# Kernel optimization log

Hardware: AMD Instinct MI355X
Metric: run time of the kernel (lower is better)

The kernel has to match this reference:

```python
import jax, jax.numpy as jnp
import numpy as np

USER_NUM = 100000
ITEM_NUM = 50000
N = USER_NUM + ITEM_NUM
D = 64
NNZ = 2400000
B = 4096
NLEVEL = 3
LEAF = 32
HID = 256
NCLS = 2
NLAYERS = 2
EPS = 0.1
TAU = 0.2


def _l2norm(x, axis=-1):
    return x / jnp.clip(jnp.linalg.norm(x, axis=axis, keepdims=True), 1e-12)


def setup_inputs():
    key = jax.random.key(0)
    ks = jax.random.split(key, 32)
    def w(k, shape):
        fan = shape[-2] if len(shape) >= 2 else shape[-1]
        return jax.random.normal(k, shape, jnp.float32) / np.sqrt(fan)
    z = lambda *s: jnp.zeros(s, jnp.float32)
    return {
        "ego_emb": w(ks[0], (N, D)),
        "gc_w": w(ks[1], (NLAYERS, D, D)), "gc_b": z(NLAYERS, D),
        "bi_w": w(ks[2], (NLAYERS, D, D)), "bi_b": z(NLAYERS, D),
        "uh_w": w(ks[3], (NLEVEL, D, D)), "uh_b": z(NLEVEL, D),
        "ih_w": w(ks[4], (NLEVEL, D, D)), "ih_b": z(NLEVEL, D),
        "ud_w1": w(ks[5], (NLEVEL, D, HID)), "ud_b1": z(NLEVEL, HID),
        "ud_w2": w(ks[6], (NLEVEL, HID, LEAF)), "ud_b2": z(NLEVEL, LEAF),
        "id_w1": w(ks[7], (NLEVEL, D, HID)), "id_b1": z(NLEVEL, HID),
        "id_w2": w(ks[8], (NLEVEL, HID, LEAF)), "id_b2": z(NLEVEL, LEAF),
        "q_w": w(ks[9], (LEAF, LEAF)), "q_b": z(LEAF),
        "k_w": w(ks[10], (LEAF, LEAF)), "k_b": z(LEAF),
        "v_w": w(ks[11], (LEAF, LEAF)), "v_b": z(LEAF),
        "dg_w1": w(ks[12], (NLEVEL * LEAF, D)), "dg_b1": z(D),
        "dg_w2": w(ks[13], (D, D)), "dg_b2": z(D),
        "pr_w": w(ks[14], (D, NCLS)), "pr_b": z(NCLS),
        "adj_vals": jax.random.uniform(ks[15], (NNZ,), jnp.float32) / 16.0,
        "hier_skills": jax.random.uniform(ks[16], (B, NLEVEL * LEAF), jnp.float32),
        "user_id": jax.random.randint(ks[17], (B,), 0, USER_NUM),
        "item_id": jax.random.randint(ks[18], (B,), 0, ITEM_NUM),
        "adj_rows": jax.random.randint(ks[19], (NNZ,), 0, N),
        "adj_cols": jax.random.randint(ks[20], (NNZ,), 0, N),
    }


def _sam(x, q_w, q_b, k_w, k_b, v_w, v_b):
    # x: [B, S, d], single-head self-attention (n_heads=1)
    d = x.shape[-1]
    q = x @ q_w + q_b
    k = x @ k_w + k_b
    v = x @ v_w + v_b
    scores = jnp.einsum('bsd,btd->bst', q, k) / jnp.sqrt(jnp.float32(d))
    attn = jax.nn.softmax(scores, axis=-1)  # softmax over key axis t
    return jnp.einsum('bst,btd->bsd', attn, v)


def _cl_loss(v1, v2):
    n1 = _l2norm(v1)
    n2 = _l2norm(v2)
    pos = jnp.exp(jnp.sum(n1 * n2, -1) / TAU)
    ttl = jnp.sum(jnp.exp(n1 @ n2.T / TAU), axis=1)
    return jnp.mean(-jnp.log(pos / ttl))


def _cl_module(recs, key):
    # recs: [L, B, LEAF]
    noise = jax.random.uniform(key, recs.shape, recs.dtype)
    recs_new = recs + jnp.sign(recs) * _l2norm(noise) * EPS
    return jnp.mean(jax.vmap(_cl_loss)(recs, recs_new))


def reference(ego_emb, gc_w, gc_b, bi_w, bi_b, uh_w, uh_b, ih_w, ih_b,
              ud_w1, ud_b1, ud_w2, ud_b2, id_w1, id_b1, id_w2, id_b2,
              q_w, q_b, k_w, k_b, v_w, v_b, dg_w1, dg_b1, dg_w2, dg_b2,
              pr_w, pr_b, adj_vals, hier_skills, user_id, item_id,
              adj_rows, adj_cols):
    # ---- NGCF propagation: sparse adj matmul + bi-interaction ----
    E = ego_emb
    E_sum = ego_emb
    for l in range(NLAYERS):
        side = jax.ops.segment_sum(adj_vals[:, None] * E[adj_cols], adj_rows,
                                   num_segments=N)  # spmm(adj_norm, E)
        sum_e = jax.nn.leaky_relu(side @ gc_w[l] + gc_b[l])
        bi_e = jax.nn.leaky_relu((E * side) @ bi_w[l] + bi_b[l])
        E = _l2norm(sum_e + bi_e)  # dropout -> identity (eval)
        E_sum = E_sum + E
    ue = E_sum[:USER_NUM][user_id]   # [B, D]
    ie = E_sum[USER_NUM:][item_id]   # [B, D]
    # ---- hierarchy projections + disentangled encoders (stacked over levels) ----
    u_reps = jnp.tanh(jnp.einsum('bd,lde->lbe', ue, uh_w) + uh_b[:, None, :])
    i_reps = jnp.tanh(jnp.einsum('bd,lde->lbe', ie, ih_w) + ih_b[:, None, :])
    u_recs = jnp.einsum('lbh,lhk->lbk',
                        jnp.tanh(jnp.einsum('lbd,ldh->lbh', u_reps, ud_w1) + ud_b1[:, None, :]),
                        ud_w2) + ud_b2[:, None, :]  # [L, B, LEAF]
    i_recs = jnp.einsum('lbh,lhk->lbk',
                        jnp.tanh(jnp.einsum('lbd,ldh->lbh', i_reps, id_w1) + id_b1[:, None, :]),
                        id_w2) + id_b2[:, None, :]
    # ---- self-attention across levels ----
    u_att = _sam(u_recs.transpose(1, 0, 2), q_w, q_b, k_w, k_b, v_w, v_b)  # [B, L, LEAF]
    i_att = _sam(i_recs.transpose(1, 0, 2), q_w, q_b, k_w, k_b, v_w, v_b)
    # ---- contrastive losses (detached in original via torch.Tensor(...)) ----
    kc = jax.random.split(jax.random.key(42), 2)
    cl = _cl_module(u_att.transpose(1, 0, 2), kc[0]) + _cl_module(i_att.transpose(1, 0, 2), kc[1])
    cl = jax.lax.stop_gradient(cl)
    # ---- diagnosis head ----
    skills = hier_skills.reshape(B, NLEVEL, LEAF)
    diag = ((jax.nn.sigmoid(u_att) - jax.nn.sigmoid(i_att)) * skills).reshape(B, NLEVEL * LEAF)
    h = jnp.tanh(diag @ dg_w1 + dg_b1) @ dg_w2 + dg_b2  # dropout -> identity (eval)
    out = jax.nn.softmax(h @ pr_w + pr_b, axis=-1)
    return (out, cl)
```

## Files before the change

### kernel.cpp

```cpp
#include <hip/hip_runtime.h>
#include <stdint.h>
#include <math.h>

#define USER_N 100000
#define NODE_N 150000
#define DD 64
#define NNZE 2400000
#define BB 4096
#define NLV 3
#define LF 32
#define HALF_SZ 196608u
#define NTILE 586
#define NSUB 8
#define SCAP 1024
#define EPB 4096
#define LCAP 5120

typedef __attribute__((ext_vector_type(8))) short bf16x8;
typedef __attribute__((ext_vector_type(4))) float f32x4;
typedef __attribute__((ext_vector_type(2))) float f32x2;

#define XCC_ID_IMM 63508

__host__ __device__ inline void tf_block(uint32_t k0, uint32_t k1, uint32_t& x0, uint32_t& x1) {
  uint32_t ks[3] = {k0, k1, k0 ^ k1 ^ 0x1BD11BDAu};
  x0 += ks[0]; x1 += ks[1];
  const int R0[4] = {13, 15, 26, 6};
  const int R1[4] = {17, 29, 16, 24};
#pragma unroll
  for (int i = 0; i < 5; ++i) {
    const int* R = (i & 1) ? R1 : R0;
#pragma unroll
    for (int j = 0; j < 4; ++j) {
      x0 += x1;
      x1 = (x1 << R[j]) | (x1 >> (32 - R[j]));
      x1 ^= x0;
    }
    x0 += ks[(i + 1) % 3];
    x1 += ks[(i + 2) % 3] + (uint32_t)(i + 1);
  }
}

__device__ inline float tf_uniform(uint32_t ka, uint32_t kb, uint32_t m) {
  uint32_t x0, x1;
  bool first = m < HALF_SZ;
  if (first) { x0 = m; x1 = m + HALF_SZ; } else { x0 = m - HALF_SZ; x1 = m; }
  tf_block(ka, kb, x0, x1);
  uint32_t bits = first ? x0 : x1;
  return __uint_as_float((bits >> 9) | 0x3f800000u) - 1.0f;
}

__device__ inline unsigned short f2bf(float x) {
  uint32_t b = __float_as_uint(x);
  return (unsigned short)((b + 0x7FFFu + ((b >> 16) & 1u)) >> 16);
}

__device__ inline unsigned char f2fp8(float x) {
  return (unsigned char)(__builtin_amdgcn_cvt_pk_fp8_f32(x, x, 0, false) & 0xFF);
}

__device__ inline void fp8_fma(float4& acc, uint2 rec, uint32_t wrd) {
  float vv = __uint_as_float(rec.y);
  f32x2 lo = __builtin_amdgcn_cvt_pk_f32_fp8((int)wrd, false);
  f32x2 hi = __builtin_amdgcn_cvt_pk_f32_fp8((int)wrd, true);
  acc.x = fmaf(vv, lo.x, acc.x);
  acc.y = fmaf(vv, lo.y, acc.y);
  acc.z = fmaf(vv, hi.x, acc.z);
  acc.w = fmaf(vv, hi.y, acc.w);
}

__global__ __launch_bounds__(256) void k_init(
    const float* __restrict__ ego, uint32_t* __restrict__ E8,
    const float* __restrict__ uh_w, const float* __restrict__ ud_w1,
    const float* __restrict__ ud_w2, const float* __restrict__ ih_w,
    const float* __restrict__ id_w1, const float* __restrict__ id_w2,
    unsigned short* __restrict__ s1t, unsigned short* __restrict__ s2t,
    unsigned short* __restrict__ s3t) {
  if (blockIdx.x < 9375) {
    int i = blockIdx.x * 256 + threadIdx.x;
    float4 v = ((const float4*)ego)[i];
    int w01 = __builtin_amdgcn_cvt_pk_fp8_f32(v.x, v.y, 0, false);
    int w = __builtin_amdgcn_cvt_pk_fp8_f32(v.z, v.w, w01, true);
    E8[i] = (uint32_t)w;
    return;
  }
  int i = (blockIdx.x - 9375) * 256 + threadIdx.x;
  if (i < 24576) {
    int sl = i >> 12, r = i & 4095, e = r >> 6, d = r & 63;
    const float* src = (sl >= 3 ? ih_w : uh_w);
    int l = sl % 3;
    s1t[i] = f2bf(src[l * 4096 + d * 64 + e]);
  } else if (i < 24576 + 98304) {
    int j = i - 24576;
    int sl = j >> 14, r = j & 16383, e = r >> 6, d = r & 63;
    const float* src = (sl >= 3 ? id_w1 : ud_w1);
    int l = sl % 3;
    s2t[j] = f2bf(src[l * 16384 + d * 256 + e]);
  } else if (i < 172032) {
    int j = i - 24576 - 98304;
    int sl = j >> 13, r = j & 8191, e = r >> 8, d = r & 255;
    const float* src = (sl >= 3 ? id_w2 : ud_w2);
    int l = sl % 3;
    s3t[j] = f2bf(src[l * 8192 + d * 32 + e]);
  }
}

__global__ __launch_bounds__(256) void k_scatter_t(const int* __restrict__ rows,
                                                   const int* __restrict__ cols,
                                                   const float* __restrict__ vals,
                                                   int* __restrict__ cursor,
                                                   uint2* __restrict__ sedge_r) {
  __shared__ int cnt[NTILE];
  __shared__ int binbase[NTILE];
  __shared__ int gbase[NTILE];
  __shared__ int partial[256];
  __shared__ uint2 staged[EPB];
  __shared__ unsigned short tileof[EPB];
  int t = threadIdx.x;
  for (int i = t; i < NTILE; i += 256) cnt[i] = 0;
  __syncthreads();
  int ebase = blockIdx.x * EPB;
  int r[16], rk[16];
#pragma unroll
  for (int j = 0; j < 16; ++j) {
    int e = ebase + j * 256 + t;
    r[j] = (e < NNZE) ? rows[e] : -1;
    rk[j] = (r[j] >= 0) ? atomicAdd(&cnt[r[j] >> 8], 1) : 0;
  }
  __syncthreads();
  int b0 = t * 3;
  int own = (b0 < NTILE) ? ((NTILE - b0 < 3) ? (NTILE - b0) : 3) : 0;
  int s0 = 0;
  for (int k = 0; k < own; ++k) s0 += cnt[b0 + k];
  partial[t] = s0;
  __syncthreads();
  for (int off = 1; off < 256; off <<= 1) {
    int add = (t >= off) ? partial[t - off] : 0;
    __syncthreads();
    partial[t] += add;
    __syncthreads();
  }
  int excl = partial[t] - s0;
  unsigned myx = __builtin_amdgcn_s_getreg(XCC_ID_IMM) & (NSUB - 1);
  {
    int run = excl;
    for (int k = 0; k < own; ++k) {
      int b = b0 + k;
      int c = cnt[b];
      binbase[b] = run;
      gbase[b] = c ? atomicAdd(&cursor[(b * NSUB + (int)myx) * 16], c) : 0;
      run += c;
    }
  }
  __syncthreads();
#pragma unroll
  for (int j = 0; j < 16; ++j) {
    if (r[j] < 0) continue;
    int e = ebase + j * 256 + t;
    int tile = r[j] >> 8;
    int pos = binbase[tile] + rk[j];
    staged[pos] = make_uint2((uint32_t)cols[e] | ((uint32_t)(r[j] & 255) << 18),
                             __float_as_uint(vals[e]));
    tileof[pos] = (unsigned short)tile;
  }
  __syncthreads();
  int nrec = NNZE - ebase;
  if (nrec > EPB) nrec = EPB;
  for (int i = t; i < nrec; i += 256) {
    int tile = tileof[i];
    int q = i - binbase[tile];
    int p = gbase[tile] + q;
    uint2 rec = staged[i];
    if (p < SCAP) {
      sedge_r[(size_t)(tile * NSUB + (int)myx) * SCAP + p] = rec;
    } else {
#pragma unroll 1
      for (int att = 1; att < NSUB; ++att) {
        int seg = tile * NSUB + (int)((myx + att) & (NSUB - 1));
        int p2 = atomicAdd(&cursor[seg * 16], 1);
        if (p2 < SCAP) { sedge_r[(size_t)seg * SCAP + p2] = rec; break; }
      }
    }
  }
}

__global__ __launch_bounds__(256) void k_sort_t(const uint2* __restrict__ sedge_r,
                                                const int* __restrict__ cursor,
                                                uint2* __restrict__ sedge,
                                                int* __restrict__ row_start) {
  __shared__ int hist[256], buf[256], curs[256];
  __shared__ int obase_s;
  __shared__ uint2 staged[LCAP];
  int t = threadIdx.x;
  int tile = blockIdx.x;
  if (t == 0) obase_s = 0;
  hist[t] = 0;
  __syncthreads();
  int ob = 0;
  for (int i = t; i < tile * NSUB; i += 256) {
    int c = cursor[i * 16];
    ob += (c < SCAP) ? c : SCAP;
  }
  if (ob) atomicAdd(&obase_s, ob);
  int segcnt[NSUB];
#pragma unroll
  for (int x = 0; x < NSUB; ++x) {
    int c = cursor[(tile * NSUB + x) * 16];
    segcnt[x] = (c < SCAP) ? c : SCAP;
  }
#pragma unroll 1
  for (int x = 0; x < NSUB; ++x) {
    const uint2* sp = sedge_r + (size_t)(tile * NSUB + x) * SCAP;
    for (int i = t; i < segcnt[x]; i += 256)
      atomicAdd(&hist[sp[i].x >> 18], 1);
  }
  __syncthreads();
  int obase = obase_s;
  int v = hist[t];
  buf[t] = v;
  __syncthreads();
  for (int off = 1; off < 256; off <<= 1) {
    int add = (t >= off) ? buf[t - off] : 0;
    __syncthreads();
    buf[t] += add;
    __syncthreads();
  }
  int total = buf[255];
  int excl = buf[t] - v;
  curs[t] = excl;
  int row = tile * 256 + t;
  if (row < NODE_N) row_start[row] = obase + excl;
  if (tile == NTILE - 1 && t == 0) row_start[NODE_N] = NNZE;
  __syncthreads();
#pragma unroll 1
  for (int x = 0; x < NSUB; ++x) {
    const uint2* sp = sedge_r + (size_t)(tile * NSUB + x) * SCAP;
    for (int i = t; i < segcnt[x]; i += 256) {
      uint2 rec = sp[i];
      int rl = rec.x >> 18;
      int p = atomicAdd(&curs[rl], 1);
      uint2 outrec = make_uint2(rec.x & 0x3FFFFu, rec.y);
      if (p < LCAP) staged[p] = outrec;
      else sedge[obase + p] = outrec;
    }
  }
  __syncthreads();
  int n = (total < LCAP) ? total : LCAP;
  for (int i = t; i < n; i += 256)
    sedge[obase + i] = staged[i];
}

__global__ __launch_bounds__(256) void k_spmm(const uint32_t* __restrict__ E8,
                                              const uint2* __restrict__ sedge,
                                              const int* __restrict__ row_start,
                                              unsigned short* __restrict__ side16,
                                              unsigned short* __restrict__ p16) {
  int r = blockIdx.x * 4 + (threadIdx.x >> 6);
  int lane = threadIdx.x & 63;
  int g = lane >> 4;
  int q = lane & 15;
  int rs = row_start[r], re = row_start[r + 1];
  float4 acc = make_float4(0.f, 0.f, 0.f, 0.f);
  int e = rs;
  for (; e + 16 <= re; e += 16) {
    uint2 e0 = sedge[e + g];
    uint2 e1 = sedge[e + 4 + g];
    uint2 e2 = sedge[e + 8 + g];
    uint2 e3 = sedge[e + 12 + g];
    uint32_t a0 = E8[(size_t)e0.x * 16 + q];
    uint32_t a1 = E8[(size_t)e1.x * 16 + q];
    uint32_t a2 = E8[(size_t)e2.x * 16 + q];
    uint32_t a3 = E8[(size_t)e3.x * 16 + q];
    fp8_fma(acc, e0, a0);
    fp8_fma(acc, e1, a1);
    fp8_fma(acc, e2, a2);
    fp8_fma(acc, e3, a3);
  }
  for (; e + 8 <= re; e += 8) {
    uint2 e0 = sedge[e + g];
    uint2 e1 = sedge[e + 4 + g];
    uint32_t a0 = E8[(size_t)e0.x * 16 + q];
    uint32_t a1 = E8[(size_t)e1.x * 16 + q];
    fp8_fma(acc, e0, a0);
    fp8_fma(acc, e1, a1);
  }
  for (; e + 4 <= re; e += 4) {
    uint2 e0 = sedge[e + g];
    uint32_t a0 = E8[(size_t)e0.x * 16 + q];
    fp8_fma(acc, e0, a0);
  }
  for (; e < re; ++e) {
    if (g == (e & 3)) {
      uint2 e0 = sedge[e];
      uint32_t a0 = E8[(size_t)e0.x * 16 + q];
      fp8_fma(acc, e0, a0);
    }
  }
#pragma unroll
  for (int off = 16; off <= 32; off <<= 1) {
    acc.x += __shfl_xor(acc.x, off, 64);
    acc.y += __shfl_xor(acc.y, off, 64);
    acc.z += __shfl_xor(acc.z, off, 64);
    acc.w += __shfl_xor(acc.w, off, 64);
  }
  if (g == 0) {
    uint32_t ew = E8[(size_t)r * 16 + q];
    f32x2 elo = __builtin_amdgcn_cvt_pk_f32_fp8((int)ew, false);
    f32x2 ehi = __builtin_amdgcn_cvt_pk_f32_fp8((int)ew, true);
    ushort4 s16, pp;
    s16.x = f2bf(acc.x); s16.y = f2bf(acc.y); s16.z = f2bf(acc.z); s16.w = f2bf(acc.w);
    pp.x = f2bf(acc.x * elo.x); pp.y = f2bf(acc.y * elo.y);
    pp.z = f2bf(acc.z * ehi.x); pp.w = f2bf(acc.w * ehi.y);
    *(ushort4*)&side16[(size_t)r * DD + q * 4] = s16;
    *(ushort4*)&p16[(size_t)r * DD + q * 4] = pp;
  }
}

__global__ __launch_bounds__(256) void k_transform(const float* __restrict__ gw,
                                                   const float* __restrict__ gb,
                                                   const float* __restrict__ bw,
                                                   const float* __restrict__ bb,
                                                   const unsigned short* __restrict__ side16,
                                                   const unsigned short* __restrict__ p16,
                                                   float* __restrict__ Eout,
                                                   unsigned char* __restrict__ E8b) {
  int t = threadIdx.x;
  int wv = t >> 6, lane = t & 63;
  int n = lane & 15, quad = lane >> 4;
  bf16x8 wg[4][2], wb[4][2];
  float gbl[4], bbl[4];
#pragma unroll
  for (int c = 0; c < 4; ++c) {
    gbl[c] = gb[c * 16 + n];
    bbl[c] = bb[c * 16 + n];
#pragma unroll
    for (int h = 0; h < 2; ++h) {
#pragma unroll
      for (int j = 0; j < 8; ++j) {
        int k = h * 32 + quad * 8 + j;
        wg[c][h][j] = (short)f2bf(gw[k * 64 + c * 16 + n]);
        wb[c][h][j] = (short)f2bf(bw[k * 64 + c * 16 + n]);
      }
    }
  }
  const f32x4 z = {0.f, 0.f, 0.f, 0.f};
  for (int tile = blockIdx.x * 4 + wv; tile < NODE_N / 16; tile += gridDim.x * 4) {
    int i0 = tile * 16;
    bf16x8 as0 = *(const bf16x8*)&side16[(size_t)(i0 + n) * DD + quad * 8];
    bf16x8 as1 = *(const bf16x8*)&side16[(size_t)(i0 + n) * DD + 32 + quad * 8];
    bf16x8 ap0 = *(const bf16x8*)&p16[(size_t)(i0 + n) * DD + quad * 8];
    bf16x8 ap1 = *(const bf16x8*)&p16[(size_t)(i0 + n) * DD + 32 + quad * 8];
    float v[4][4];
    float sq0 = 0.f, sq1 = 0.f, sq2 = 0.f, sq3 = 0.f;
#pragma unroll
    for (int c = 0; c < 4; ++c) {
      f32x4 ag = __builtin_amdgcn_mfma_f32_16x16x32_bf16(as0, wg[c][0], z, 0, 0, 0);
      ag = __builtin_amdgcn_mfma_f32_16x16x32_bf16(as1, wg[c][1], ag, 0, 0, 0);
      f32x4 ab = __builtin_amdgcn_mfma_f32_16x16x32_bf16(ap0, wb[c][0], z, 0, 0, 0);
      ab = __builtin_amdgcn_mfma_f32_16x16x32_bf16(ap1, wb[c][1], ab, 0, 0, 0);
#pragma unroll
      for (int r = 0; r < 4; ++r) {
        float a1 = ag[r] + gbl[c];
        a1 = (a1 > 0.f) ? a1 : 0.01f * a1;
        float a2 = ab[r] + bbl[c];
        a2 = (a2 > 0.f) ? a2 : 0.01f * a2;
        float vv = a1 + a2;
        v[c][r] = vv;
        if (r == 0) sq0 += vv * vv;
        else if (r == 1) sq1 += vv * vv;
        else if (r == 2) sq2 += vv * vv;
        else sq3 += vv * vv;
      }
    }
#pragma unroll
    for (int off = 1; off < 16; off <<= 1) {
      sq0 += __shfl_xor(sq0, off, 64);
      sq1 += __shfl_xor(sq1, off, 64);
      sq2 += __shfl_xor(sq2, off, 64);
      sq3 += __shfl_xor(sq3, off, 64);
    }
    float inv0 = 1.f / fmaxf(sqrtf(sq0), 1e-12f);
    float inv1 = 1.f / fmaxf(sqrtf(sq1), 1e-12f);
    float inv2 = 1.f / fmaxf(sqrtf(sq2), 1e-12f);
    float inv3 = 1.f / fmaxf(sqrtf(sq3), 1e-12f);
#pragma unroll
    for (int c = 0; c < 4; ++c) {
      float vn0 = v[c][0] * inv0;
      float vn1 = v[c][1] * inv1;
      float vn2 = v[c][2] * inv2;
      float vn3 = v[c][3] * inv3;
      size_t o0 = (size_t)(i0 + quad * 4 + 0) * DD + c * 16 + n;
      size_t o1 = o0 + DD, o2 = o1 + DD, o3 = o2 + DD;
      Eout[o0] = vn0; Eout[o1] = vn1; Eout[o2] = vn2; Eout[o3] = vn3;
      E8b[o0] = f2fp8(vn0); E8b[o1] = f2fp8(vn1);
      E8b[o2] = f2fp8(vn2); E8b[o3] = f2fp8(vn3);
    }
  }
}

__global__ __launch_bounds__(128) void k_gather(const float* __restrict__ ego,
                                                const float* __restrict__ E1,
                                                const float* __restrict__ E2,
                                                const int* __restrict__ uid,
                                                const int* __restrict__ iid,
                                                unsigned short* __restrict__ ue16,
                                                unsigned short* __restrict__ ie16) {
  int b = blockIdx.x, t = threadIdx.x;
  if (t < 64) {
    size_t o = (size_t)uid[b] * 64 + t;
    ue16[(size_t)b * 64 + t] = f2bf(ego[o] + E1[o] + E2[o]);
  } else {
    int d = t - 64;
    size_t o = (size_t)(USER_N + iid[b]) * 64 + d;
    ie16[(size_t)b * 64 + d] = f2bf(ego[o] + E1[o] + E2[o]);
  }
}

__global__ __launch_bounds__(256) void k_encoder5(
    const unsigned short* __restrict__ ue16, const unsigned short* __restrict__ ie16,
    const unsigned short* __restrict__ s1t, const unsigned short* __restrict__ s2t,
    const unsigned short* __restrict__ s3t,
    const float* __restrict__ uh_b, const float* __restrict__ ud_b1,
    const float* __restrict__ ud_b2, const float* __restrict__ ih_b,
    const float* __restrict__ id_b1, const float* __restrict__ id_b2,
    float* __restrict__ recs_u, float* __restrict__ recs_i) {
  __shared__ unsigned short R1[32][64];
  __shared__ unsigned short T[32][256];
  int t = threadIdx.x;
  int w = t >> 6, lane = t & 63;
  int n = lane & 15, quad = lane >> 4;
  int trow = w & 1;
  int cg = w >> 1;
  int r0 = blockIdx.x * 32;
  int l = blockIdx.y, side = blockIdx.z;
  int sl = side * 3 + l;
  const unsigned short* x16 = side ? ie16 : ue16;
  const float* hb = side ? ih_b : uh_b;
  const float* bb1 = side ? id_b1 : ud_b1;
  const float* bb2 = side ? id_b2 : ud_b2;
  float* recs = side ? recs_i : recs_u;
  const f32x4 z = {0.f, 0.f, 0.f, 0.f};

  {
    const unsigned short* xr = &x16[(size_t)(r0 + trow * 16 + n) * 64];
    bf16x8 a0 = *(const bf16x8*)&xr[quad * 8];
    bf16x8 a1 = *(const bf16x8*)&xr[32 + quad * 8];
    const unsigned short* Wt = s1t + (size_t)sl * 4096;
#pragma unroll
    for (int cc = 0; cc < 2; ++cc) {
      int cb = cg * 2 + cc;
      bf16x8 wb0 = *(const bf16x8*)&Wt[(size_t)(cb * 16 + n) * 64 + quad * 8];
      bf16x8 wb1 = *(const bf16x8*)&Wt[(size_t)(cb * 16 + n) * 64 + 32 + quad * 8];
      f32x4 acc = __builtin_amdgcn_mfma_f32_16x16x32_bf16(a0, wb0, z, 0, 0, 0);
      acc = __builtin_amdgcn_mfma_f32_16x16x32_bf16(a1, wb1, acc, 0, 0, 0);
      float bias = hb[l * 64 + cb * 16 + n];
#pragma unroll
      for (int r = 0; r < 4; ++r)
        R1[trow * 16 + quad * 4 + r][cb * 16 + n] = f2bf(tanhf(acc[r] + bias));
    }
  }
  __syncthreads();

  {
    bf16x8 a0 = *(const bf16x8*)&R1[trow * 16 + n][quad * 8];
    bf16x8 a1 = *(const bf16x8*)&R1[trow * 16 + n][32 + quad * 8];
    const unsigned short* Wt = s2t + (size_t)sl * 16384;
#pragma unroll
    for (int cc = 0; cc < 8; ++cc) {
      int cb = cg * 8 + cc;
      bf16x8 wb0 = *(const bf16x8*)&Wt[(size_t)(cb * 16 + n) * 64 + quad * 8];
      bf16x8 wb1 = *(const bf16x8*)&Wt[(size_t)(cb * 16 + n) * 64 + 32 + quad * 8];
      f32x4 acc = __builtin_amdgcn_mfma_f32_16x16x32_bf16(a0, wb0, z, 0, 0, 0);
      acc = __builtin_amdgcn_mfma_f32_16x16x32_bf16(a1, wb1, acc, 0, 0, 0);
      float bias = bb1[l * 256 + cb * 16 + n];
#pragma unroll
      for (int r = 0; r < 4; ++r)
        T[trow * 16 + quad * 4 + r][cb * 16 + n] = f2bf(tanhf(acc[r] + bias));
    }
  }
  __syncthreads();

  {
    const unsigned short* Wt = s3t + (size_t)sl * 8192;
    f32x4 acc = z;
#pragma unroll
    for (int h = 0; h < 8; ++h) {
      bf16x8 a = *(const bf16x8*)&T[trow * 16 + n][h * 32 + quad * 8];
      bf16x8 b = *(const bf16x8*)&Wt[(size_t)(cg * 16 + n) * 256 + h * 32 + quad * 8];
      acc = __builtin_amdgcn_mfma_f32_16x16x32_bf16(a, b, acc, 0, 0, 0);
    }
    float bias = bb2[l * 32 + cg * 16 + n];
#pragma unroll
    for (int r = 0; r < 4; ++r)
      recs[((size_t)l * BB + (r0 + trow * 16 + quad * 4 + r)) * 32 + cg * 16 + n] =
          acc[r] + bias;
  }
}

__global__ __launch_bounds__(256) void k_attn(const float* __restrict__ recs_u,
                                              const float* __restrict__ recs_i,
                                              const float* __restrict__ qw, const float* __restrict__ qb,
                                              const float* __restrict__ kw, const float* __restrict__ kb,
                                              const float* __restrict__ vw, const float* __restrict__ vb,
                                              float* __restrict__ att_u,
                                              float* __restrict__ att_i) {
  const float* recs = blockIdx.y ? recs_i : recs_u;
  float* att = blockIdx.y ? att_i : att_u;
  int t = threadIdx.x;
  int b = blockIdx.x * 8 + (t >> 5);
  int d = t & 31;
  float x0 = recs[((size_t)0 * BB + b) * 32 + d];
  float x1 = recs[((size_t)1 * BB + b) * 32 + d];
  float x2 = recs[((size_t)2 * BB + b) * 32 + d];
  float q0 = qb[d], q1 = q0, q2 = q0;
  float c0 = kb[d], c1 = c0, c2 = c0;
  float v0 = vb[d], v1 = v0, v2 = v0;
#pragma unroll 4
  for (int kk = 0; kk < 32; ++kk) {
    float xa = __shfl(x0, kk, 32);
    float xb = __shfl(x1, kk, 32);
    float xc = __shfl(x2, kk, 32);
    float wq = qw[kk * 32 + d], wk = kw[kk * 32 + d], wv = vw[kk * 32 + d];
    q0 += xa * wq; q1 += xb * wq; q2 += xc * wq;
    c0 += xa * wk; c1 += xb * wk; c2 += xc * wk;
    v0 += xa * wv; v1 += xb * wv; v2 += xc * wv;
  }
  float qs[3] = {q0, q1, q2}, ks[3] = {c0, c1, c2}, vs[3] = {v0, v1, v2};
  float sc[3][3];
#pragma unroll
  for (int s = 0; s < 3; ++s)
#pragma unroll
    for (int u = 0; u < 3; ++u) {
      float p = qs[s] * ks[u];
#pragma unroll
      for (int off = 16; off; off >>= 1) p += __shfl_xor(p, off, 32);
      sc[s][u] = p * 0.17677669529663687f;
    }
#pragma unroll
  for (int s = 0; s < 3; ++s) {
    float m = fmaxf(sc[s][0], fmaxf(sc[s][1], sc[s][2]));
    float e0 = __expf(sc[s][0] - m), e1 = __expf(sc[s][1] - m), e2 = __expf(sc[s][2] - m);
    float inv = 1.f / (e0 + e1 + e2);
    att[(size_t)b * 96 + s * 32 + d] = (e0 * vs[0] + e1 * vs[1] + e2 * vs[2]) * inv;
  }
}

__global__ __launch_bounds__(256) void k_noise(const float* __restrict__ att_u,
                                               const float* __restrict__ att_i,
                                               uint32_t ku0, uint32_t ku1, uint32_t ki0, uint32_t ki1,
                                               unsigned short* __restrict__ n1b,
                                               unsigned short* __restrict__ n2b,
                                               float* __restrict__ posdot) {
  int t = threadIdx.x;
  int g = blockIdx.x * 8 + (t >> 5);
  int k = t & 31;
  int side = g / (NLV * BB);
  int rem = g - side * (NLV * BB);
  int l = rem >> 12;
  int b = rem & 4095;
  const float* att = side ? att_i : att_u;
  uint32_t ka = side ? ki0 : ku0;
  uint32_t kb = side ? ki1 : ku1;
  float r = att[(size_t)b * 96 + l * 32 + k];
  float ss = r * r;
#pragma unroll
  for (int off = 16; off; off >>= 1) ss += __shfl_xor(ss, off, 32);
  float v1 = r / fmaxf(sqrtf(ss), 1e-12f);
  uint32_t m = ((uint32_t)(l * BB + b)) * 32u + (uint32_t)k;
  float u = tf_uniform(ka, kb, m);
  float us = u * u;
#pragma unroll
  for (int off = 16; off; off >>= 1) us += __shfl_xor(us, off, 32);
  float un = u / fmaxf(sqrtf(us), 1e-12f);
  float sgn = (r > 0.f) ? 1.f : ((r < 0.f) ? -1.f : 0.f);
  float rn = r + sgn * un * 0.1f;
  float s2 = rn * rn;
#pragma unroll
  for (int off = 16; off; off >>= 1) s2 += __shfl_xor(s2, off, 32);
  float v2 = rn / fmaxf(sqrtf(s2), 1e-12f);
  float pd = v1 * v2;
#pragma unroll
  for (int off = 16; off; off >>= 1) pd += __shfl_xor(pd, off, 32);
  size_t o = (size_t)g * 32 + k;
  n1b[o] = f2bf(v1);
  n2b[o] = f2bf(v2);
  if (k == 0) posdot[g] = pd;
}

__global__ __launch_bounds__(256) void k_ttl(const unsigned short* __restrict__ n1b,
                                             const unsigned short* __restrict__ n2b,
                                             float* __restrict__ ttl) {
  int t = threadIdx.x;
  int wv = t >> 6, lane = t & 63;
  int sl = blockIdx.x >> 6;
  int istripe = blockIdx.x & 63;
  int i0 = istripe * 64 + wv * 16;
  const unsigned short* ab = n1b + (size_t)sl * BB * 32;
  const unsigned short* bb = n2b + (size_t)sl * BB * 32;
  int m = lane & 15, quad = lane >> 4;
  bf16x8 afrag = *(const bf16x8*)&ab[(size_t)(i0 + m) * 32 + quad * 8];
  float r0a = 0.f, r1a = 0.f, r2a = 0.f, r3a = 0.f;
  f32x4 z = {0.f, 0.f, 0.f, 0.f};
  for (int jt = 0; jt < 256; jt += 4) {
    bf16x8 b0 = *(const bf16x8*)&bb[((size_t)((jt + 0) * 16 + m)) * 32 + quad * 8];
    bf16x8 b1 = *(const bf16x8*)&bb[((size_t)((jt + 1) * 16 + m)) * 32 + quad * 8];
    bf16x8 b2 = *(const bf16x8*)&bb[((size_t)((jt + 2) * 16 + m)) * 32 + quad * 8];
    bf16x8 b3 = *(const bf16x8*)&bb[((size_t)((jt + 3) * 16 + m)) * 32 + quad * 8];
    f32x4 s0 = __builtin_amdgcn_mfma_f32_16x16x32_bf16(afrag, b0, z, 0, 0, 0);
    f32x4 s1 = __builtin_amdgcn_mfma_f32_16x16x32_bf16(afrag, b1, z, 0, 0, 0);
    f32x4 s2 = __builtin_amdgcn_mfma_f32_16x16x32_bf16(afrag, b2, z, 0, 0, 0);
    f32x4 s3 = __builtin_amdgcn_mfma_f32_16x16x32_bf16(afrag, b3, z, 0, 0, 0);
    r0a += __expf(s0.x * 5.f) + __expf(s1.x * 5.f) + __expf(s2.x * 5.f) + __expf(s3.x * 5.f);
    r1a += __expf(s0.y * 5.f) + __expf(s1.y * 5.f) + __expf(s2.y * 5.f) + __expf(s3.y * 5.f);
    r2a += __expf(s0.z * 5.f) + __expf(s1.z * 5.f) + __expf(s2.z * 5.f) + __expf(s3.z * 5.f);
    r3a += __expf(s0.w * 5.f) + __expf(s1.w * 5.f) + __expf(s2.w * 5.f) + __expf(s3.w * 5.f);
  }
#pragma unroll
  for (int off = 1; off < 16; off <<= 1) {
    r0a += __shfl_xor(r0a, off, 64);
    r1a += __shfl_xor(r1a, off, 64);
    r2a += __shfl_xor(r2a, off, 64);
    r3a += __shfl_xor(r3a, off, 64);
  }
  if (m == 0) {
    int rbase = sl * BB + i0 + quad * 4;
    ttl[rbase + 0] = r0a;
    ttl[rbase + 1] = r1a;
    ttl[rbase + 2] = r2a;
    ttl[rbase + 3] = r3a;
  }
}

__global__ __launch_bounds__(1024) void k_clred(const float* __restrict__ ttl,
                                                const float* __restrict__ posdot,
                                                float* __restrict__ outp) {
  __shared__ float red[1024];
  int t = threadIdx.x;
  float a = 0.f;
  for (int idx = t; idx < 6 * BB; idx += 1024)
    a += logf(ttl[idx]) - posdot[idx] * 5.0f;
  red[t] = a;
  __syncthreads();
  for (int off = 512; off; off >>= 1) {
    if (t < off) red[t] += red[t + off];
    __syncthreads();
  }
  if (t == 0) outp[2 * BB] = red[0] * (1.f / 12288.f);
}

__global__ __launch_bounds__(256) void k_head(const float* __restrict__ att_u,
                                              const float* __restrict__ att_i,
                                              const float* __restrict__ skills,
                                              const float* __restrict__ w1, const float* __restrict__ b1,
                                              const float* __restrict__ w2, const float* __restrict__ b2,
                                              const float* __restrict__ pw, const float* __restrict__ pb,
                                              float* __restrict__ outp) {
  __shared__ float diag[4][96], t1[4][64];
  int t = threadIdx.x;
  int w = t >> 6, lane = t & 63;
  int b = blockIdx.x * 4 + w;
  for (int j = lane; j < 96; j += 64) {
    float su = 1.f / (1.f + __expf(-att_u[(size_t)b * 96 + j]));
    float si = 1.f / (1.f + __expf(-att_i[(size_t)b * 96 + j]));
    diag[w][j] = (su - si) * skills[(size_t)b * 96 + j];
  }
  __syncthreads();
  float a = b1[lane];
#pragma unroll 8
  for (int j = 0; j < 96; ++j) a += diag[w][j] * w1[j * 64 + lane];
  t1[w][lane] = tanhf(a);
  __syncthreads();
  float h = b2[lane];
#pragma unroll 8
  for (int kk = 0; kk < 64; ++kk) h += t1[w][kk] * w2[kk * 64 + lane];
  float p0 = h * pw[lane * 2 + 0];
  float p1 = h * pw[lane * 2 + 1];
#pragma unroll
  for (int off = 32; off; off >>= 1) {
    p0 += __shfl_xor(p0, off, 64);
    p1 += __shfl_xor(p1, off, 64);
  }
  if (lane == 0) {
    float l0 = p0 + pb[0], l1 = p1 + pb[1];
    float m = fmaxf(l0, l1);
    float e0 = __expf(l0 - m), e1 = __expf(l1 - m);
    float inv = 1.f / (e0 + e1);
    outp[(size_t)b * 2 + 0] = e0 * inv;
    outp[(size_t)b * 2 + 1] = e1 * inv;
  }
}

extern "C" void kernel_launch(void* const* d_in, const int* in_sizes, int n_in,
                              void* d_out, int out_size, void* d_ws, size_t ws_size,
                              hipStream_t stream) {
  const float* ego    = (const float*)d_in[0];
  const float* gc_w   = (const float*)d_in[1];
  const float* gc_b   = (const float*)d_in[2];
  const float* bi_w   = (const float*)d_in[3];
  const float* bi_b   = (const float*)d_in[4];
  const float* uh_w   = (const float*)d_in[5];
  const float* uh_b   = (const float*)d_in[6];
  const float* ih_w   = (const float*)d_in[7];
  const float* ih_b   = (const float*)d_in[8];
  const float* ud_w1  = (const float*)d_in[9];
  const float* ud_b1  = (const float*)d_in[10];
  const float* ud_w2  = (const float*)d_in[11];
  const float* ud_b2  = (const float*)d_in[12];
  const float* id_w1  = (const float*)d_in[13];
  const float* id_b1  = (const float*)d_in[14];
  const float* id_w2  = (const float*)d_in[15];
  const float* id_b2  = (const float*)d_in[16];
  const float* q_w    = (const float*)d_in[17];
  const float* q_b    = (const float*)d_in[18];
  const float* k_w    = (const float*)d_in[19];
  const float* k_b    = (const float*)d_in[20];
  const float* v_w    = (const float*)d_in[21];
  const float* v_b    = (const float*)d_in[22];
  const float* dg_w1  = (const float*)d_in[23];
  const float* dg_b1  = (const float*)d_in[24];
  const float* dg_w2  = (const float*)d_in[25];
  const float* dg_b2  = (const float*)d_in[26];
  const float* pr_w   = (const float*)d_in[27];
  const float* pr_b   = (const float*)d_in[28];
  const float* adj_vals = (const float*)d_in[29];
  const float* skills = (const float*)d_in[30];
  const int* user_id  = (const int*)d_in[31];
  const int* item_id  = (const int*)d_in[32];
  const int* adj_rows = (const int*)d_in[33];
  const int* adj_cols = (const int*)d_in[34];
  float* outp = (float*)d_out;

  char* w = (char*)d_ws;
  auto alloc = [&](size_t bytes) -> char* {
    char* p = w;
    w += (bytes + 255) & ~(size_t)255;
    return p;
  };
  float* E1     = (float*)alloc((size_t)NODE_N * DD * 4);
  float* E2     = (float*)alloc((size_t)NODE_N * DD * 4);
  uint32_t* E8  = (uint32_t*)alloc((size_t)NODE_N * DD);
  unsigned short* side16 = (unsigned short*)alloc((size_t)NODE_N * DD * 2);
  unsigned short* p16    = (unsigned short*)alloc((size_t)NODE_N * DD * 2);
  uint2* sedge_r= (uint2*)alloc((size_t)NTILE * NSUB * SCAP * 8);
  uint2* sedge  = (uint2*)alloc((size_t)NNZE * 8);
  int*   cursor = (int*)  alloc((size_t)NTILE * NSUB * 16 * 4);
  int*   row_start = (int*)alloc((size_t)(NODE_N + 1) * 4);
  float* posdot = (float*)alloc((size_t)6 * BB * 4);
  float* ttl    = (float*)alloc((size_t)6 * BB * 4);
  unsigned short* s1t = (unsigned short*)alloc((size_t)24576 * 2);
  unsigned short* s2t = (unsigned short*)alloc((size_t)98304 * 2);
  unsigned short* s3t = (unsigned short*)alloc((size_t)49152 * 2);

  char* ap = (char*)sedge_r;
  auto alias = [&](size_t bytes) -> char* {
    char* p = ap;
    ap += (bytes + 255) & ~(size_t)255;
    return p;
  };
  unsigned short* ue16 = (unsigned short*)alias((size_t)BB * 64 * 2);
  unsigned short* ie16 = (unsigned short*)alias((size_t)BB * 64 * 2);
  float* recs_u = (float*)alias((size_t)NLV * BB * 32 * 4);
  float* recs_i = (float*)alias((size_t)NLV * BB * 32 * 4);
  float* att_u  = (float*)alias((size_t)BB * 96 * 4);
  float* att_i  = (float*)alias((size_t)BB * 96 * 4);
  unsigned short* n1b = (unsigned short*)alias((size_t)6 * BB * 32 * 2);
  unsigned short* n2b = (unsigned short*)alias((size_t)6 * BB * 32 * 2);

  uint32_t a0 = 0, a1 = 2, b0 = 1, b1 = 3;
  tf_block(0u, 42u, a0, a1);
  tf_block(0u, 42u, b0, b1);
  uint32_t ku0 = a0, ku1 = b0;
  uint32_t ki0 = a1, ki1 = b1;

  (void)hipMemsetAsync(cursor, 0, (size_t)NTILE * NSUB * 16 * 4, stream);

  k_init<<<9375 + 672, 256, 0, stream>>>(ego, E8, uh_w, ud_w1, ud_w2,
                                         ih_w, id_w1, id_w2, s1t, s2t, s3t);
  k_scatter_t<<<(NNZE + EPB - 1) / EPB, 256, 0, stream>>>(adj_rows, adj_cols, adj_vals,
                                                          cursor, sedge_r);
  k_sort_t<<<NTILE, 256, 0, stream>>>(sedge_r, cursor, sedge, row_start);

  float* Ebufs[2] = {E1, E2};
  for (int l = 0; l < 2; ++l) {
    k_spmm<<<37500, 256, 0, stream>>>(E8, sedge, row_start, side16, p16);
    k_transform<<<1172, 256, 0, stream>>>(gc_w + l * 4096, gc_b + l * 64,
                                          bi_w + l * 4096, bi_b + l * 64,
                                          side16, p16, Ebufs[l], (unsigned char*)E8);
  }

  k_gather<<<4096, 128, 0, stream>>>(ego, E1, E2, user_id, item_id, ue16, ie16);

  dim3 ge(128, 3, 2);
  k_encoder5<<<ge, 256, 0, stream>>>(ue16, ie16, s1t, s2t, s3t,
                                     uh_b, ud_b1, ud_b2, ih_b, id_b1, id_b2,
                                     recs_u, recs_i);

  dim3 ga(512, 2);
  k_attn<<<ga, 256, 0, stream>>>(recs_u, recs_i, q_w, q_b, k_w, k_b, v_w, v_b,
                                 att_u, att_i);

  k_noise<<<3072, 256, 0, stream>>>(att_u, att_i, ku0, ku1, ki0, ki1, n1b, n2b, posdot);

  k_ttl<<<384, 256, 0, stream>>>(n1b, n2b, ttl);
  k_clred<<<1, 1024, 0, stream>>>(ttl, posdot, outp);

  k_head<<<1024, 256, 0, stream>>>(att_u, att_i, skills, dg_w1, dg_b1, dg_w2, dg_b2,
                                   pr_w, pr_b, outp);
}
```

Before: 524.6 us.

## Fuse gather, noise and CL reduction kernels and fold memset into init

Folds the cursor memset and a new CL accumulator reset into extra blocks of the init kernel. The user/item embedding gather moves into the encoder, and the noise/normalisation step moves into the attention kernel. The final CL reduction moves into k_ttl via atomics with a last-block-done counter. This removes four launches and several small intermediate buffers, in exchange for atomic float accumulation order nondeterminism and redundant gathers across the three level blocks.

```diff
diff --git a/kernel.cpp b/kernel.cpp
--- a/kernel.cpp
+++ b/kernel.cpp
@@ -75,7 +75,14 @@
     const float* __restrict__ ud_w2, const float* __restrict__ ih_w,
     const float* __restrict__ id_w1, const float* __restrict__ id_w2,
     unsigned short* __restrict__ s1t, unsigned short* __restrict__ s2t,
-    unsigned short* __restrict__ s3t) {
+    unsigned short* __restrict__ s3t, int* __restrict__ cursor,
+    float* __restrict__ clbuf) {
+  if (blockIdx.x >= 10047) {
+    int i = (blockIdx.x - 10047) * 256 + threadIdx.x;
+    if (i < NTILE * NSUB * 16) cursor[i] = 0;
+    if (i == 0) { clbuf[0] = 0.f; ((int*)clbuf)[1] = 0; }
+    return;
+  }
   if (blockIdx.x < 9375) {
     int i = blockIdx.x * 256 + threadIdx.x;
     float4 v = ((const float4*)ego)[i];
@@ -398,32 +405,17 @@
   }
 }
 
-__global__ __launch_bounds__(128) void k_gather(const float* __restrict__ ego,
-                                                const float* __restrict__ E1,
-                                                const float* __restrict__ E2,
-                                                const int* __restrict__ uid,
-                                                const int* __restrict__ iid,
-                                                unsigned short* __restrict__ ue16,
-                                                unsigned short* __restrict__ ie16) {
-  int b = blockIdx.x, t = threadIdx.x;
-  if (t < 64) {
-    size_t o = (size_t)uid[b] * 64 + t;
-    ue16[(size_t)b * 64 + t] = f2bf(ego[o] + E1[o] + E2[o]);
-  } else {
-    int d = t - 64;
-    size_t o = (size_t)(USER_N + iid[b]) * 64 + d;
-    ie16[(size_t)b * 64 + d] = f2bf(ego[o] + E1[o] + E2[o]);
-  }
-}
-
-__global__ __launch_bounds__(256) void k_encoder5(
-    const unsigned short* __restrict__ ue16, const unsigned short* __restrict__ ie16,
+__global__ __launch_bounds__(256) void k_encoder6(
+    const float* __restrict__ ego, const float* __restrict__ E1,
+    const float* __restrict__ E2, const int* __restrict__ uid,
+    const int* __restrict__ iid,
     const unsigned short* __restrict__ s1t, const unsigned short* __restrict__ s2t,
     const unsigned short* __restrict__ s3t,
     const float* __restrict__ uh_b, const float* __restrict__ ud_b1,
     const float* __restrict__ ud_b2, const float* __restrict__ ih_b,
     const float* __restrict__ id_b1, const float* __restrict__ id_b2,
     float* __restrict__ recs_u, float* __restrict__ recs_i) {
+  __shared__ unsigned short X[32][72];
   __shared__ unsigned short R1[32][64];
   __shared__ unsigned short T[32][256];
   int t = threadIdx.x;
@@ -434,7 +426,6 @@
   int r0 = blockIdx.x * 32;
   int l = blockIdx.y, side = blockIdx.z;
   int sl = side * 3 + l;
-  const unsigned short* x16 = side ? ie16 : ue16;
   const float* hb = side ? ih_b : uh_b;
   const float* bb1 = side ? id_b1 : ud_b1;
   const float* bb2 = side ? id_b2 : ud_b2;
@@ -442,9 +433,21 @@
   const f32x4 z = {0.f, 0.f, 0.f, 0.f};
 
   {
-    const unsigned short* xr = &x16[(size_t)(r0 + trow * 16 + n) * 64];
-    bf16x8 a0 = *(const bf16x8*)&xr[quad * 8];
-    bf16x8 a1 = *(const bf16x8*)&xr[32 + quad * 8];
+    int row = t >> 3;
+    int c0 = (t & 7) * 8;
+    int node = side ? (USER_N + iid[r0 + row]) : uid[r0 + row];
+    const float* pe = ego + (size_t)node * 64 + c0;
+    const float* p1 = E1 + (size_t)node * 64 + c0;
+    const float* p2 = E2 + (size_t)node * 64 + c0;
+#pragma unroll
+    for (int j = 0; j < 8; ++j)
+      X[row][c0 + j] = f2bf(pe[j] + p1[j] + p2[j]);
+  }
+  __syncthreads();
+
+  {
+    bf16x8 a0 = *(const bf16x8*)&X[trow * 16 + n][quad * 8];
+    bf16x8 a1 = *(const bf16x8*)&X[trow * 16 + n][32 + quad * 8];
     const unsigned short* Wt = s1t + (size_t)sl * 4096;
 #pragma unroll
     for (int cc = 0; cc < 2; ++cc) {
@@ -497,15 +500,21 @@
   }
 }
 
-__global__ __launch_bounds__(256) void k_attn(const float* __restrict__ recs_u,
-                                              const float* __restrict__ recs_i,
-                                              const float* __restrict__ qw, const float* __restrict__ qb,
-                                              const float* __restrict__ kw, const float* __restrict__ kb,
-                                              const float* __restrict__ vw, const float* __restrict__ vb,
-                                              float* __restrict__ att_u,
-                                              float* __restrict__ att_i) {
-  const float* recs = blockIdx.y ? recs_i : recs_u;
-  float* att = blockIdx.y ? att_i : att_u;
+__global__ __launch_bounds__(256) void k_attnz(const float* __restrict__ recs_u,
+                                               const float* __restrict__ recs_i,
+                                               const float* __restrict__ qw, const float* __restrict__ qb,
+                                               const float* __restrict__ kw, const float* __restrict__ kb,
+                                               const float* __restrict__ vw, const float* __restrict__ vb,
+                                               uint32_t ku0, uint32_t ku1, uint32_t ki0, uint32_t ki1,
+                                               float* __restrict__ att_u, float* __restrict__ att_i,
+                                               unsigned short* __restrict__ n1b,
+                                               unsigned short* __restrict__ n2b,
+                                               float* __restrict__ posdot) {
+  int side = blockIdx.y;
+  const float* recs = side ? recs_i : recs_u;
+  float* att = side ? att_i : att_u;
+  uint32_t ka = side ? ki0 : ku0;
+  uint32_t kb2 = side ? ki1 : ku1;
   int t = threadIdx.x;
   int b = blockIdx.x * 8 + (t >> 5);
   int d = t & 31;
@@ -541,55 +550,41 @@
     float m = fmaxf(sc[s][0], fmaxf(sc[s][1], sc[s][2]));
     float e0 = __expf(sc[s][0] - m), e1 = __expf(sc[s][1] - m), e2 = __expf(sc[s][2] - m);
     float inv = 1.f / (e0 + e1 + e2);
-    att[(size_t)b * 96 + s * 32 + d] = (e0 * vs[0] + e1 * vs[1] + e2 * vs[2]) * inv;
-  }
-}
-
-__global__ __launch_bounds__(256) void k_noise(const float* __restrict__ att_u,
-                                               const float* __restrict__ att_i,
-                                               uint32_t ku0, uint32_t ku1, uint32_t ki0, uint32_t ki1,
-                                               unsigned short* __restrict__ n1b,
-                                               unsigned short* __restrict__ n2b,
-                                               float* __restrict__ posdot) {
-  int t = threadIdx.x;
-  int g = blockIdx.x * 8 + (t >> 5);
-  int k = t & 31;
-  int side = g / (NLV * BB);
-  int rem = g - side * (NLV * BB);
-  int l = rem >> 12;
-  int b = rem & 4095;
-  const float* att = side ? att_i : att_u;
-  uint32_t ka = side ? ki0 : ku0;
-  uint32_t kb = side ? ki1 : ku1;
-  float r = att[(size_t)b * 96 + l * 32 + k];
-  float ss = r * r;
-#pragma unroll
-  for (int off = 16; off; off >>= 1) ss += __shfl_xor(ss, off, 32);
-  float v1 = r / fmaxf(sqrtf(ss), 1e-12f);
-  uint32_t m = ((uint32_t)(l * BB + b)) * 32u + (uint32_t)k;
-  float u = tf_uniform(ka, kb, m);
-  float us = u * u;
-#pragma unroll
-  for (int off = 16; off; off >>= 1) us += __shfl_xor(us, off, 32);
-  float un = u / fmaxf(sqrtf(us), 1e-12f);
-  float sgn = (r > 0.f) ? 1.f : ((r < 0.f) ? -1.f : 0.f);
-  float rn = r + sgn * un * 0.1f;
-  float s2 = rn * rn;
-#pragma unroll
-  for (int off = 16; off; off >>= 1) s2 += __shfl_xor(s2, off, 32);
-  float v2 = rn / fmaxf(sqrtf(s2), 1e-12f);
-  float pd = v1 * v2;
-#pragma unroll
-  for (int off = 16; off; off >>= 1) pd += __shfl_xor(pd, off, 32);
-  size_t o = (size_t)g * 32 + k;
-  n1b[o] = f2bf(v1);
-  n2b[o] = f2bf(v2);
-  if (k == 0) posdot[g] = pd;
+    float r = (e0 * vs[0] + e1 * vs[1] + e2 * vs[2]) * inv;
+    att[(size_t)b * 96 + s * 32 + d] = r;
+    float ss = r * r;
+#pragma unroll
+    for (int off = 16; off; off >>= 1) ss += __shfl_xor(ss, off, 32);
+    float nv1 = r / fmaxf(sqrtf(ss), 1e-12f);
+    uint32_t mm = ((uint32_t)(s * BB + b)) * 32u + (uint32_t)d;
+    float u = tf_uniform(ka, kb2, mm);
+    float us = u * u;
+#pragma unroll
+    for (int off = 16; off; off >>= 1) us += __shfl_xor(us, off, 32);
+    float un = u / fmaxf(sqrtf(us), 1e-12f);
+    float sgn = (r > 0.f) ? 1.f : ((r < 0.f) ? -1.f : 0.f);
+    float rn = r + sgn * un * 0.1f;
+    float s2 = rn * rn;
+#pragma unroll
+    for (int off = 16; off; off >>= 1) s2 += __shfl_xor(s2, off, 32);
+    float nv2 = rn / fmaxf(sqrtf(s2), 1e-12f);
+    float pd = nv1 * nv2;
+#pragma unroll
+    for (int off = 16; off; off >>= 1) pd += __shfl_xor(pd, off, 32);
+    int g = side * (NLV * BB) + s * BB + b;
+    size_t o = (size_t)g * 32 + d;
+    n1b[o] = f2bf(nv1);
+    n2b[o] = f2bf(nv2);
+    if (d == 0) posdot[g] = pd;
+  }
 }
 
 __global__ __launch_bounds__(256) void k_ttl(const unsigned short* __restrict__ n1b,
                                              const unsigned short* __restrict__ n2b,
-                                             float* __restrict__ ttl) {
+                                             const float* __restrict__ posdot,
+                                             float* __restrict__ clbuf,
+                                             float* __restrict__ outp) {
+  __shared__ float ws[4];
   int t = threadIdx.x;
   int wv = t >> 6, lane = t & 63;
   int sl = blockIdx.x >> 6;
@@ -622,30 +617,29 @@
     r2a += __shfl_xor(r2a, off, 64);
     r3a += __shfl_xor(r3a, off, 64);
   }
+  float part = 0.f;
   if (m == 0) {
     int rbase = sl * BB + i0 + quad * 4;
-    ttl[rbase + 0] = r0a;
-    ttl[rbase + 1] = r1a;
-    ttl[rbase + 2] = r2a;
-    ttl[rbase + 3] = r3a;
-  }
-}
-
-__global__ __launch_bounds__(1024) void k_clred(const float* __restrict__ ttl,
-                                                const float* __restrict__ posdot,
-                                                float* __restrict__ outp) {
-  __shared__ float red[1024];
-  int t = threadIdx.x;
-  float a = 0.f;
-  for (int idx = t; idx < 6 * BB; idx += 1024)
-    a += logf(ttl[idx]) - posdot[idx] * 5.0f;
-  red[t] = a;
-  __syncthreads();
-  for (int off = 512; off; off >>= 1) {
-    if (t < off) red[t] += red[t + off];
-    __syncthreads();
-  }
-  if (t == 0) outp[2 * BB] = red[0] * (1.f / 12288.f);
+    part = (logf(r0a) - posdot[rbase + 0] * 5.0f)
+         + (logf(r1a) - posdot[rbase + 1] * 5.0f)
+         + (logf(r2a) - posdot[rbase + 2] * 5.0f)
+         + (logf(r3a) - posdot[rbase + 3] * 5.0f);
+  }
+#pragma unroll
+  for (int off = 1; off < 64; off <<= 1)
+    part += __shfl_xor(part, off, 64);
+  if (lane == 0) ws[wv] = part;
+  __syncthreads();
+  if (t == 0) {
+    float blk = ws[0] + ws[1] + ws[2] + ws[3];
+    atomicAdd(&clbuf[0], blk);
+    __threadfence();
+    int done = atomicAdd((int*)&clbuf[1], 1);
+    if (done == 383) {
+      float total = atomicAdd(&clbuf[0], 0.0f);
+      outp[2 * BB] = total * (1.f / 12288.f);
+    }
+  }
 }
 
 __global__ __launch_bounds__(256) void k_head(const float* __restrict__ att_u,
@@ -746,7 +740,7 @@
   int*   cursor = (int*)  alloc((size_t)NTILE * NSUB * 16 * 4);
   int*   row_start = (int*)alloc((size_t)(NODE_N + 1) * 4);
   float* posdot = (float*)alloc((size_t)6 * BB * 4);
-  float* ttl    = (float*)alloc((size_t)6 * BB * 4);
+  float* clbuf  = (float*)alloc(256);
   unsigned short* s1t = (unsigned short*)alloc((size_t)24576 * 2);
   unsigned short* s2t = (unsigned short*)alloc((size_t)98304 * 2);
   unsigned short* s3t = (unsigned short*)alloc((size_t)49152 * 2);
@@ -757,8 +751,6 @@
     ap += (bytes + 255) & ~(size_t)255;
     return p;
   };
-  unsigned short* ue16 = (unsigned short*)alias((size_t)BB * 64 * 2);
-  unsigned short* ie16 = (unsigned short*)alias((size_t)BB * 64 * 2);
   float* recs_u = (float*)alias((size_t)NLV * BB * 32 * 4);
   float* recs_i = (float*)alias((size_t)NLV * BB * 32 * 4);
   float* att_u  = (float*)alias((size_t)BB * 96 * 4);
@@ -772,10 +764,9 @@
   uint32_t ku0 = a0, ku1 = b0;
   uint32_t ki0 = a1, ki1 = b1;
 
-  (void)hipMemsetAsync(cursor, 0, (size_t)NTILE * NSUB * 16 * 4, stream);
-
-  k_init<<<9375 + 672, 256, 0, stream>>>(ego, E8, uh_w, ud_w1, ud_w2,
-                                         ih_w, id_w1, id_w2, s1t, s2t, s3t);
+  k_init<<<10341, 256, 0, stream>>>(ego, E8, uh_w, ud_w1, ud_w2,
+                                    ih_w, id_w1, id_w2, s1t, s2t, s3t,
+                                    cursor, clbuf);
   k_scatter_t<<<(NNZE + EPB - 1) / EPB, 256, 0, stream>>>(adj_rows, adj_cols, adj_vals,
                                                           cursor, sedge_r);
   k_sort_t<<<NTILE, 256, 0, stream>>>(sedge_r, cursor, sedge, row_start);
@@ -788,21 +779,18 @@
                                           side16, p16, Ebufs[l], (unsigned char*)E8);
   }
 
-  k_gather<<<4096, 128, 0, stream>>>(ego, E1, E2, user_id, item_id, ue16, ie16);
-
   dim3 ge(128, 3, 2);
-  k_encoder5<<<ge, 256, 0, stream>>>(ue16, ie16, s1t, s2t, s3t,
+  k_encoder6<<<ge, 256, 0, stream>>>(ego, E1, E2, user_id, item_id,
+                                     s1t, s2t, s3t,
                                      uh_b, ud_b1, ud_b2, ih_b, id_b1, id_b2,
                                      recs_u, recs_i);
 
   dim3 ga(512, 2);
-  k_attn<<<ga, 256, 0, stream>>>(recs_u, recs_i, q_w, q_b, k_w, k_b, v_w, v_b,
-                                 att_u, att_i);
-
-  k_noise<<<3072, 256, 0, stream>>>(att_u, att_i, ku0, ku1, ki0, ki1, n1b, n2b, posdot);
-
-  k_ttl<<<384, 256, 0, stream>>>(n1b, n2b, ttl);
-  k_clred<<<1, 1024, 0, stream>>>(ttl, posdot, outp);
+  k_attnz<<<ga, 256, 0, stream>>>(recs_u, recs_i, q_w, q_b, k_w, k_b, v_w, v_b,
+                                  ku0, ku1, ki0, ki1,
+                                  att_u, att_i, n1b, n2b, posdot);
+
+  k_ttl<<<384, 256, 0, stream>>>(n1b, n2b, posdot, clbuf, outp);
 
   k_head<<<1024, 256, 0, stream>>>(att_u, att_i, skills, dg_w1, dg_b1, dg_w2, dg_b2,
                                    pr_w, pr_b, outp);
```

After: 515.1 us. Within noise of the previous version (-1.8%).
